# Optimization experiments

Measured on AMD Instinct MI355X. Metric: run time of the kernel, lower is better.

The kernel has to match this reference:

```python
import jax, jax.numpy as jnp
import numpy as np

ALPHA = 10.0
BETA = 2.0


def _l2norm(x):
    return x / jnp.linalg.norm(x, axis=1, keepdims=True)


def setup_inputs() -> dict:
    key = jax.random.key(0)
    k1, k2, k3 = jax.random.split(key, 3)
    n, C, d = 4096, 10000, 2048
    inputs = _l2norm(jax.random.normal(k1, (n, d), dtype=jnp.float32))
    kernel = _l2norm(jax.random.normal(k2, (C, d), dtype=jnp.float32))
    targets = jax.random.randint(k3, (n,), 0, C, dtype=jnp.int64 if jax.config.jax_enable_x64 else jnp.int32)
    return {"inputs": inputs, "targets": targets, "kernel": kernel}


def reference(inputs, targets, kernel):
    n = inputs.shape[0]
    C = kernel.shape[0]
    rows = jnp.arange(n)

    # cos_theta uses a detached kernel (no grad through this GEMM in original)
    cos = jnp.clip(inputs @ jax.lax.stop_gradient(kernel).T, -1.0, 1.0)  # [n, C]

    # phi_i = <inputs_i, kernel[targets_i]> - beta  (grad flows to kernel here)
    phi = jnp.sum(inputs * kernel[targets], axis=1) - BETA  # [n]

    pos_cos = cos[rows, targets]  # cos_theta at target columns, [n]
    mean_proxy_pos = pos_cos.sum() / n
    mean_proxy_neg = (cos.sum() - pos_cos.sum()) / (n * (C - 1))

    # output = cos_theta with target entries replaced by phi
    output = cos.at[rows, targets].set(phi)  # [n, C]
    onehot = jax.nn.one_hot(targets, C, dtype=output.dtype)

    loss_pos = phi  # sum(output * onehot, axis=1)
    loss_neg = jnp.log(jnp.sum(jnp.exp(output * ALPHA) * (1.0 - onehot), axis=1))  # [n]
    loss_mask = (jnp.max(output, axis=1) - phi) > 0.0
    per_sample = -loss_pos + loss_neg / ALPHA
    denom = jnp.maximum(loss_mask.sum(), 1).astype(per_sample.dtype)
    loss = jnp.sum(jnp.where(loss_mask, per_sample, 0.0)) / denom

    pred = jnp.argmax(output, axis=1)
    prec = jnp.mean((pred == targets).astype(jnp.float32))

    sim = inputs @ inputs.T  # [n, n]
    sim_label = (targets[:, None] == targets[None, :]).astype(sim.dtype)
    pos_cnt = sim_label.sum()
    neg_cnt = (n * n) - pos_cnt
    mean_pos_sim = jnp.sum(sim * sim_label) / pos_cnt
    mean_neg_sim = jnp.sum(sim * (1.0 - sim_label)) / neg_cnt

    return (loss, prec, mean_proxy_pos, mean_proxy_neg, mean_pos_sim, mean_neg_sim)
```

## Files before the change

### kernel.cpp

```cpp
#include <hip/hip_runtime.h>
#include <hip/hip_bf16.h>

#define NROWS 4096
#define NCLS  10000
#define DIM   2048
#define DIMB  1024
#define ALPHA_F 10.0f
#define BETA_F  2.0f
#define FP4_SCALE 64.0f
#define INVQ (1.0f / (FP4_SCALE * FP4_SCALE))
#define NMAIN_BLK 2560
#define NSIM_BLK  528

typedef float f32x4 __attribute__((ext_vector_type(4)));
typedef int   i32x4 __attribute__((ext_vector_type(4)));
typedef int   i32x8 __attribute__((ext_vector_type(8)));

__global__ void cast_fp4_kernel(const float* __restrict__ X, const float* __restrict__ Kn,
                                unsigned int* __restrict__ dA, unsigned int* __restrict__ dB,
                                int nA8, int nT8) {
  int stride = gridDim.x * blockDim.x;
  for (int i = blockIdx.x * blockDim.x + threadIdx.x; i < nT8; i += stride) {
    const float* src; unsigned int* dst; int j;
    if (i < nA8) { src = X; dst = dA; j = i; } else { src = Kn; dst = dB; j = i - nA8; }
    float4 a = reinterpret_cast<const float4*>(src)[2 * j];
    float4 b = reinterpret_cast<const float4*>(src)[2 * j + 1];
    float v[8] = {a.x, a.y, a.z, a.w, b.x, b.y, b.z, b.w};
    unsigned int w = 0;
#pragma unroll
    for (int q = 0; q < 8; ++q) {
      float s = v[q] * FP4_SCALE;
      float av = fabsf(s);
      unsigned int code = (unsigned)(av > 0.25f) + (av > 0.75f) + (av > 1.25f)
                        + (av > 1.75f) + (av > 2.5f) + (av > 3.5f) + (av > 5.0f);
      code |= (s < 0.f) ? 8u : 0u;
      w |= code << (4 * q);
    }
    dst[j] = w;
  }
}

__global__ void gather_dot_kernel(const float* __restrict__ X, const float* __restrict__ Kn,
                                  const int* __restrict__ tgt, float* __restrict__ dotv) {
  int gtid = blockIdx.x * blockDim.x + threadIdx.x;
  int wave = gtid >> 6;
  int lane = threadIdx.x & 63;
  if (wave >= NROWS) return;
  const float* xr = X + (size_t)wave * DIM;
  const float* kr = Kn + (size_t)tgt[wave] * DIM;
  float s = 0.f;
#pragma unroll
  for (int it = 0; it < DIM / 256; ++it) {
    int k = lane * 4 + it * 256;
    float4 a = *reinterpret_cast<const float4*>(xr + k);
    float4 b = *reinterpret_cast<const float4*>(kr + k);
    s += a.x * b.x + a.y * b.y + a.z * b.z + a.w * b.w;
  }
#pragma unroll
  for (int off = 32; off > 0; off >>= 1) s += __shfl_down(s, off);
  if (lane == 0) dotv[wave] = s;
}


#define AS1 const __attribute__((address_space(1))) void*
#define AS3 __attribute__((address_space(3))) void*

__global__ __launch_bounds__(256, 4)
void gemm_kernel(const unsigned char* __restrict__ A,
                 const unsigned char* __restrict__ Bm,
                 const float* __restrict__ dotv,
                 const int* __restrict__ tgt,
                 float* __restrict__ S1, float* __restrict__ Eacc,
                 float* __restrict__ CNT, float* __restrict__ simAcc) {
  __shared__ unsigned char lds[2 * 16384];

  const int tid  = threadIdx.x;
  const int lane = tid & 63;
  const int wid  = tid >> 6;
  const int wr   = wid >> 1;
  const int wc   = wid & 1;
  const int fr   = lane & 15;
  const int kg   = lane >> 4;

  const int lin = blockIdx.x;
  const bool isMain = lin < NMAIN_BLK;
  int rowTile, colTile, nB;
  const unsigned char* B;
  if (isMain) {
    int swz = (lin & 7) * 320 + (lin >> 3);
    colTile = swz / 32;
    rowTile = swz % 32;
    B = Bm; nB = NCLS;
  } else {
    int l2 = lin - NMAIN_BLK;
    int swz = (l2 & 7) * 66 + (l2 >> 3);
    int r = 0;
    while ((r + 1) * (r + 2) / 2 <= swz) ++r;
    rowTile = r;
    colTile = swz - r * (r + 1) / 2;
    B = A; nB = NROWS;
  }
  const int rowBase = rowTile * 128;
  const int colBase = colTile * 128;

  const int l0  = tid >> 3;
  const int sp  = tid & 7;
  const int lg8 = sp ^ (l0 & 7);
  const int shi = lg8 >> 2, sc16 = lg8 & 3;
  const int rA0 = rowBase + 2 * l0 + shi;
  const int rA1 = rA0 + 64;
  int cB0 = colBase + 2 * l0 + shi;      if (cB0 > nB - 1) cB0 = nB - 1;
  int cB1 = colBase + 64 + 2 * l0 + shi; if (cB1 > nB - 1) cB1 = nB - 1;
  const unsigned char* pA0 = A + (size_t)rA0 * DIMB + sc16 * 16;
  const unsigned char* pA1 = A + (size_t)rA1 * DIMB + sc16 * 16;
  const unsigned char* pB0 = B + (size_t)cB0 * DIMB + sc16 * 16;
  const unsigned char* pB1 = B + (size_t)cB1 * DIMB + sc16 * 16;
  const int dOff = l0 * 128 + sp * 16;

#define STAGE_TILE(BUF, KT)                                                     \
  { int ko_ = (KT) * 64;                                                        \
    unsigned char* d_ = lds + (BUF) * 16384 + dOff;                             \
    __builtin_amdgcn_global_load_lds((AS1)(pA0 + ko_), (AS3)(d_),          16, 0, 0); \
    __builtin_amdgcn_global_load_lds((AS1)(pA1 + ko_), (AS3)(d_ + 4096),   16, 0, 0); \
    __builtin_amdgcn_global_load_lds((AS1)(pB0 + ko_), (AS3)(d_ + 8192),   16, 0, 0); \
    __builtin_amdgcn_global_load_lds((AS1)(pB1 + ko_), (AS3)(d_ + 12288),  16, 0, 0); }

  int offA[4], offB[4];
#pragma unroll
  for (int m2 = 0; m2 < 4; ++m2) {
    int lr = wr * 64 + m2 * 16 + fr;
    int l = lr >> 1;
    offA[m2] = l * 128 + ((((lr & 1) * 4 + kg) ^ (l & 7)) << 4);
  }
#pragma unroll
  for (int n2 = 0; n2 < 4; ++n2) {
    int lc = wc * 64 + n2 * 16 + fr;
    int l = lc >> 1;
    offB[n2] = 8192 + l * 128 + ((((lc & 1) * 4 + kg) ^ (l & 7)) << 4);
  }

  f32x4 acc[4][4];
  const f32x4 zero = {0.f, 0.f, 0.f, 0.f};
#pragma unroll
  for (int m = 0; m < 4; ++m)
#pragma unroll
    for (int n = 0; n < 4; ++n) acc[m][n] = zero;

  STAGE_TILE(0, 0);
  __syncthreads();

#pragma unroll 1
  for (int kt = 0; kt < 16; ++kt) {
    const int buf = kt & 1;
    const int ktn = (kt < 15) ? kt + 1 : 15;
    STAGE_TILE(buf ^ 1, ktn);
    const unsigned char* lb = lds + buf * 16384;
    i32x8 afr[4], bfr[4];
#pragma unroll
    for (int m2 = 0; m2 < 4; ++m2) {
      i32x4 v_ = *reinterpret_cast<const i32x4*>(lb + offA[m2]);
      afr[m2][0] = v_[0]; afr[m2][1] = v_[1]; afr[m2][2] = v_[2]; afr[m2][3] = v_[3];
      afr[m2][4] = 0; afr[m2][5] = 0; afr[m2][6] = 0; afr[m2][7] = 0;
    }
#pragma unroll
    for (int n2 = 0; n2 < 4; ++n2) {
      i32x4 v_ = *reinterpret_cast<const i32x4*>(lb + offB[n2]);
      bfr[n2][0] = v_[0]; bfr[n2][1] = v_[1]; bfr[n2][2] = v_[2]; bfr[n2][3] = v_[3];
      bfr[n2][4] = 0; bfr[n2][5] = 0; bfr[n2][6] = 0; bfr[n2][7] = 0;
    }
    __builtin_amdgcn_s_setprio(1);
#pragma unroll
    for (int m2 = 0; m2 < 4; ++m2)
#pragma unroll
      for (int n2 = 0; n2 < 4; ++n2)
        acc[m2][n2] = __builtin_amdgcn_mfma_scale_f32_16x16x128_f8f6f4(
            afr[m2], bfr[n2], acc[m2][n2], 4, 4, 0, 127, 0, 127);
    __builtin_amdgcn_s_setprio(0);
    __syncthreads();
  }

  __syncthreads();

  if (isMain) {
    float* shPhi = reinterpret_cast<float*>(lds);
    if (tid < 128) shPhi[tid] = dotv[rowBase + tid] - BETA_F;
    __syncthreads();
#pragma unroll
    for (int m = 0; m < 4; ++m) {
#pragma unroll
      for (int j = 0; j < 4; ++j) {
        int rl = wr * 64 + m * 16 + kg * 4 + j;
        float ph = shPhi[rl];
        float s1 = 0.f, ee = 0.f, ct = 0.f;
#pragma unroll
        for (int n = 0; n < 4; ++n) {
          int gcol = colBase + wc * 64 + n * 16 + fr;
          float c = acc[m][n][j] * INVQ;
          c = fminf(fmaxf(c, -1.f), 1.f);
          if (gcol < NCLS) {
            s1 += c;
            ee += __expf(ALPHA_F * c);
            ct += (c > ph) ? 1.f : 0.f;
          }
        }
#pragma unroll
        for (int o = 1; o < 16; o <<= 1) {
          s1 += __shfl_xor(s1, o);
          ee += __shfl_xor(ee, o);
          ct += __shfl_xor(ct, o);
        }
        if (fr == 0) {
          int grow = rowBase + rl;
          atomicAdd(&S1[grow], s1);
          atomicAdd(&Eacc[grow], ee);
          atomicAdd(&CNT[grow], ct);
        }
      }
    }
  } else {
    const float wgt = (rowTile == colTile) ? 1.f : 2.f;
    int* shT = reinterpret_cast<int*>(lds);
    float* redbuf = reinterpret_cast<float*>(lds + 4096);
    if (tid < 128) shT[tid] = tgt[rowBase + tid];
    else if (tid < 256) shT[tid] = tgt[colBase + (tid - 128)];
    __syncthreads();
    float ps = 0.f, als = 0.f, pc = 0.f;
#pragma unroll
    for (int m = 0; m < 4; ++m) {
#pragma unroll
      for (int j = 0; j < 4; ++j) {
        int rl = wr * 64 + m * 16 + kg * 4 + j;
        int tr = shT[rl];
#pragma unroll
        for (int n = 0; n < 4; ++n) {
          int cl = wc * 64 + n * 16 + fr;
          float c = acc[m][n][j] * INVQ;
          als += c;
          if (tr == shT[128 + cl]) { ps += c; pc += 1.f; }
        }
      }
    }
#pragma unroll
    for (int o = 1; o < 64; o <<= 1) {
      ps  += __shfl_xor(ps, o);
      als += __shfl_xor(als, o);
      pc  += __shfl_xor(pc, o);
    }
    if (lane == 0) {
      redbuf[wid * 3 + 0] = ps;
      redbuf[wid * 3 + 1] = als;
      redbuf[wid * 3 + 2] = pc;
    }
    __syncthreads();
    if (tid == 0) {
      float p = 0.f, a = 0.f, c2 = 0.f;
      for (int w = 0; w < 4; ++w) {
        p += redbuf[w * 3 + 0];
        a += redbuf[w * 3 + 1];
        c2 += redbuf[w * 3 + 2];
      }
      atomicAdd(&simAcc[0], wgt * p);
      atomicAdd(&simAcc[1], wgt * a);
      atomicAdd(&simAcc[2], wgt * c2);
    }
  }
}

__global__ void finalize_kernel(const float* __restrict__ dotv, const float* __restrict__ S1,
                                const float* __restrict__ Eacc, const float* __restrict__ CNT,
                                const float* __restrict__ simAcc, float* __restrict__ out) {
  __shared__ float sh[5][256];
  int tid = threadIdx.x;
  float sum_posc = 0.f, sum_s1 = 0.f, loss_sum = 0.f, mask_cnt = 0.f, correct = 0.f;
  for (int i = tid; i < NROWS; i += 256) {
    float d = dotv[i];
    float posc = fminf(fmaxf(d, -1.f), 1.f);
    float phi = d - BETA_F;
    sum_posc += posc;
    sum_s1 += S1[i];
    float e = Eacc[i] - __expf(ALPHA_F * posc);
    float cexcl = CNT[i] - 1.f;
    float per = -phi + __logf(e) / ALPHA_F;
    if (cexcl > 0.5f) { loss_sum += per; mask_cnt += 1.f; }
    else correct += 1.f;
  }
  sh[0][tid] = sum_posc; sh[1][tid] = sum_s1; sh[2][tid] = loss_sum;
  sh[3][tid] = mask_cnt; sh[4][tid] = correct;
  __syncthreads();
  for (int s = 128; s > 0; s >>= 1) {
    if (tid < s)
      for (int q = 0; q < 5; ++q) sh[q][tid] += sh[q][tid + s];
    __syncthreads();
  }
  if (tid == 0) {
    float posS = sh[0][0], s1S = sh[1][0], lossS = sh[2][0], maskS = sh[3][0], corr = sh[4][0];
    out[0] = lossS / fmaxf(maskS, 1.f);
    out[1] = corr / (float)NROWS;
    out[2] = posS / (float)NROWS;
    out[3] = (s1S - posS) / ((float)NROWS * (float)(NCLS - 1));
    float pos = simAcc[0], all = simAcc[1], pcnt = simAcc[2];
    out[4] = pos / pcnt;
    out[5] = (all - pos) / ((float)NROWS * (float)NROWS - pcnt);
  }
}

extern "C" void kernel_launch(void* const* d_in, const int* in_sizes, int n_in,
                              void* d_out, int out_size, void* d_ws, size_t ws_size,
                              hipStream_t stream) {
  const float* X  = (const float*)d_in[0];
  const int*   tg = (const int*)d_in[1];
  const float* Kn = (const float*)d_in[2];
  float* out = (float*)d_out;

  char* w = (char*)d_ws;
  unsigned char* f4A = (unsigned char*)w;
  unsigned char* f4B = f4A + (size_t)NROWS * DIMB;
  float* dotv   = (float*)(w + (size_t)NROWS * DIMB + (size_t)NCLS * DIMB);
  float* S1     = dotv + NROWS;
  float* Eacc   = S1 + NROWS;
  float* CNT    = Eacc + NROWS;
  float* simAcc = CNT + NROWS;

  hipMemsetAsync(S1, 0, (3 * NROWS + 4) * sizeof(float), stream);

  const int nA8 = NROWS * DIM / 8, nT8 = nA8 + NCLS * DIM / 8;
  cast_fp4_kernel<<<2048, 256, 0, stream>>>(X, Kn, (unsigned int*)f4A,
                                            (unsigned int*)f4B, nA8, nT8);
  gather_dot_kernel<<<NROWS / 4, 256, 0, stream>>>(X, Kn, tg, dotv);

  gemm_kernel<<<NMAIN_BLK + NSIM_BLK, 256, 0, stream>>>(
      f4A, f4B, dotv, tg, S1, Eacc, CNT, simAcc);

  finalize_kernel<<<1, 256, 0, stream>>>(dotv, S1, Eacc, CNT, simAcc, out);
}
```

Before: 149.2 us.

## Fuse prep kernels, trim main grid, pack reductions, widen finalize

Merges the FP4 cast and gather-dot kernels into one launch, which saves a kernel launch and lets the two run concurrently. Shrinks the main GEMM grid from 2560 to 2528 blocks (79 column tiles × 32 row tiles cover 10112 ≥ 10000 columns) to drop fully out-of-range tiles. Hoists zero-initialisation of the fragment upper halves out of the k-loop. Packs the row sum and count into one float for the shuffle reduction, cutting one of the three shuffle chains at some risk to float precision. Runs finalize with 1024 threads instead of 256.

```diff
diff --git a/kernel.cpp b/kernel.cpp
--- a/kernel.cpp
+++ b/kernel.cpp
@@ -9,56 +9,56 @@
 #define BETA_F  2.0f
 #define FP4_SCALE 64.0f
 #define INVQ (1.0f / (FP4_SCALE * FP4_SCALE))
-#define NMAIN_BLK 2560
+#define NMAIN_BLK 2528
 #define NSIM_BLK  528
 
 typedef float f32x4 __attribute__((ext_vector_type(4)));
 typedef int   i32x4 __attribute__((ext_vector_type(4)));
 typedef int   i32x8 __attribute__((ext_vector_type(8)));
 
-__global__ void cast_fp4_kernel(const float* __restrict__ X, const float* __restrict__ Kn,
-                                unsigned int* __restrict__ dA, unsigned int* __restrict__ dB,
-                                int nA8, int nT8) {
-  int stride = gridDim.x * blockDim.x;
-  for (int i = blockIdx.x * blockDim.x + threadIdx.x; i < nT8; i += stride) {
-    const float* src; unsigned int* dst; int j;
-    if (i < nA8) { src = X; dst = dA; j = i; } else { src = Kn; dst = dB; j = i - nA8; }
-    float4 a = reinterpret_cast<const float4*>(src)[2 * j];
-    float4 b = reinterpret_cast<const float4*>(src)[2 * j + 1];
-    float v[8] = {a.x, a.y, a.z, a.w, b.x, b.y, b.z, b.w};
-    unsigned int w = 0;
-#pragma unroll
-    for (int q = 0; q < 8; ++q) {
-      float s = v[q] * FP4_SCALE;
-      float av = fabsf(s);
-      unsigned int code = (unsigned)(av > 0.25f) + (av > 0.75f) + (av > 1.25f)
-                        + (av > 1.75f) + (av > 2.5f) + (av > 3.5f) + (av > 5.0f);
-      code |= (s < 0.f) ? 8u : 0u;
-      w |= code << (4 * q);
-    }
-    dst[j] = w;
-  }
-}
-
-__global__ void gather_dot_kernel(const float* __restrict__ X, const float* __restrict__ Kn,
-                                  const int* __restrict__ tgt, float* __restrict__ dotv) {
-  int gtid = blockIdx.x * blockDim.x + threadIdx.x;
-  int wave = gtid >> 6;
-  int lane = threadIdx.x & 63;
-  if (wave >= NROWS) return;
-  const float* xr = X + (size_t)wave * DIM;
-  const float* kr = Kn + (size_t)tgt[wave] * DIM;
-  float s = 0.f;
-#pragma unroll
-  for (int it = 0; it < DIM / 256; ++it) {
-    int k = lane * 4 + it * 256;
-    float4 a = *reinterpret_cast<const float4*>(xr + k);
-    float4 b = *reinterpret_cast<const float4*>(kr + k);
-    s += a.x * b.x + a.y * b.y + a.z * b.z + a.w * b.w;
-  }
-#pragma unroll
-  for (int off = 32; off > 0; off >>= 1) s += __shfl_down(s, off);
-  if (lane == 0) dotv[wave] = s;
+__global__ void prep_kernel(const float* __restrict__ X, const float* __restrict__ Kn,
+                            const int* __restrict__ tgt,
+                            unsigned int* __restrict__ dA, unsigned int* __restrict__ dB,
+                            float* __restrict__ dotv, int nA8, int nT8) {
+  if (blockIdx.x < 2048) {
+    int stride = 2048 * blockDim.x;
+    for (int i = blockIdx.x * blockDim.x + threadIdx.x; i < nT8; i += stride) {
+      const float* src; unsigned int* dst; int j;
+      if (i < nA8) { src = X; dst = dA; j = i; } else { src = Kn; dst = dB; j = i - nA8; }
+      float4 a = reinterpret_cast<const float4*>(src)[2 * j];
+      float4 b = reinterpret_cast<const float4*>(src)[2 * j + 1];
+      float v[8] = {a.x, a.y, a.z, a.w, b.x, b.y, b.z, b.w};
+      unsigned int w = 0;
+#pragma unroll
+      for (int q = 0; q < 8; ++q) {
+        float s = v[q] * FP4_SCALE;
+        float av = fabsf(s);
+        unsigned int code = (unsigned)(av > 0.25f) + (av > 0.75f) + (av > 1.25f)
+                          + (av > 1.75f) + (av > 2.5f) + (av > 3.5f) + (av > 5.0f);
+        code |= (s < 0.f) ? 8u : 0u;
+        w |= code << (4 * q);
+      }
+      dst[j] = w;
+    }
+  } else {
+    int gtid = (blockIdx.x - 2048) * blockDim.x + threadIdx.x;
+    int wave = gtid >> 6;
+    int lane = threadIdx.x & 63;
+    if (wave >= NROWS) return;
+    const float* xr = X + (size_t)wave * DIM;
+    const float* kr = Kn + (size_t)tgt[wave] * DIM;
+    float s = 0.f;
+#pragma unroll
+    for (int it = 0; it < DIM / 256; ++it) {
+      int k = lane * 4 + it * 256;
+      float4 a = *reinterpret_cast<const float4*>(xr + k);
+      float4 b = *reinterpret_cast<const float4*>(kr + k);
+      s += a.x * b.x + a.y * b.y + a.z * b.z + a.w * b.w;
+    }
+#pragma unroll
+    for (int off = 32; off > 0; off >>= 1) s += __shfl_down(s, off);
+    if (lane == 0) dotv[wave] = s;
+  }
 }
 
 
@@ -87,7 +87,7 @@
   int rowTile, colTile, nB;
   const unsigned char* B;
   if (isMain) {
-    int swz = (lin & 7) * 320 + (lin >> 3);
+    int swz = (lin & 7) * 316 + (lin >> 3);
     colTile = swz / 32;
     rowTile = swz % 32;
     B = Bm; nB = NCLS;
@@ -146,6 +146,13 @@
 #pragma unroll
     for (int n = 0; n < 4; ++n) acc[m][n] = zero;
 
+  i32x8 afr[4], bfr[4];
+#pragma unroll
+  for (int q = 0; q < 4; ++q) {
+#pragma unroll
+    for (int e = 0; e < 8; ++e) { afr[q][e] = 0; bfr[q][e] = 0; }
+  }
+
   STAGE_TILE(0, 0);
   __syncthreads();
 
@@ -155,18 +162,15 @@
     const int ktn = (kt < 15) ? kt + 1 : 15;
     STAGE_TILE(buf ^ 1, ktn);
     const unsigned char* lb = lds + buf * 16384;
-    i32x8 afr[4], bfr[4];
 #pragma unroll
     for (int m2 = 0; m2 < 4; ++m2) {
       i32x4 v_ = *reinterpret_cast<const i32x4*>(lb + offA[m2]);
       afr[m2][0] = v_[0]; afr[m2][1] = v_[1]; afr[m2][2] = v_[2]; afr[m2][3] = v_[3];
-      afr[m2][4] = 0; afr[m2][5] = 0; afr[m2][6] = 0; afr[m2][7] = 0;
     }
 #pragma unroll
     for (int n2 = 0; n2 < 4; ++n2) {
       i32x4 v_ = *reinterpret_cast<const i32x4*>(lb + offB[n2]);
       bfr[n2][0] = v_[0]; bfr[n2][1] = v_[1]; bfr[n2][2] = v_[2]; bfr[n2][3] = v_[3];
-      bfr[n2][4] = 0; bfr[n2][5] = 0; bfr[n2][6] = 0; bfr[n2][7] = 0;
     }
     __builtin_amdgcn_s_setprio(1);
 #pragma unroll
@@ -203,17 +207,19 @@
             ct += (c > ph) ? 1.f : 0.f;
           }
         }
+        float pk = s1 + ct * 4096.0f;
 #pragma unroll
         for (int o = 1; o < 16; o <<= 1) {
-          s1 += __shfl_xor(s1, o);
+          pk += __shfl_xor(pk, o);
           ee += __shfl_xor(ee, o);
-          ct += __shfl_xor(ct, o);
         }
         if (fr == 0) {
           int grow = rowBase + rl;
-          atomicAdd(&S1[grow], s1);
+          float ctv = rintf(pk * (1.0f / 4096.0f));
+          float s1v = pk - ctv * 4096.0f;
+          atomicAdd(&S1[grow], s1v);
           atomicAdd(&Eacc[grow], ee);
-          atomicAdd(&CNT[grow], ct);
+          atomicAdd(&CNT[grow], ctv);
         }
       }
     }
@@ -269,10 +275,10 @@
 __global__ void finalize_kernel(const float* __restrict__ dotv, const float* __restrict__ S1,
                                 const float* __restrict__ Eacc, const float* __restrict__ CNT,
                                 const float* __restrict__ simAcc, float* __restrict__ out) {
-  __shared__ float sh[5][256];
+  __shared__ float sh[5][1024];
   int tid = threadIdx.x;
   float sum_posc = 0.f, sum_s1 = 0.f, loss_sum = 0.f, mask_cnt = 0.f, correct = 0.f;
-  for (int i = tid; i < NROWS; i += 256) {
+  for (int i = tid; i < NROWS; i += 1024) {
     float d = dotv[i];
     float posc = fminf(fmaxf(d, -1.f), 1.f);
     float phi = d - BETA_F;
@@ -287,7 +293,7 @@
   sh[0][tid] = sum_posc; sh[1][tid] = sum_s1; sh[2][tid] = loss_sum;
   sh[3][tid] = mask_cnt; sh[4][tid] = correct;
   __syncthreads();
-  for (int s = 128; s > 0; s >>= 1) {
+  for (int s = 512; s > 0; s >>= 1) {
     if (tid < s)
       for (int q = 0; q < 5; ++q) sh[q][tid] += sh[q][tid + s];
     __syncthreads();
@@ -324,12 +330,11 @@
   hipMemsetAsync(S1, 0, (3 * NROWS + 4) * sizeof(float), stream);
 
   const int nA8 = NROWS * DIM / 8, nT8 = nA8 + NCLS * DIM / 8;
-  cast_fp4_kernel<<<2048, 256, 0, stream>>>(X, Kn, (unsigned int*)f4A,
-                                            (unsigned int*)f4B, nA8, nT8);
-  gather_dot_kernel<<<NROWS / 4, 256, 0, stream>>>(X, Kn, tg, dotv);
+  prep_kernel<<<3072, 256, 0, stream>>>(X, Kn, tg, (unsigned int*)f4A,
+                                        (unsigned int*)f4B, dotv, nA8, nT8);
 
   gemm_kernel<<<NMAIN_BLK + NSIM_BLK, 256, 0, stream>>>(
       f4A, f4B, dotv, tg, S1, Eacc, CNT, simAcc);
 
-  finalize_kernel<<<1, 256, 0, stream>>>(dotv, S1, Eacc, CNT, simAcc, out);
+  finalize_kernel<<<1, 1024, 0, stream>>>(dotv, S1, Eacc, CNT, simAcc, out);
 }
```

Result: faster. 134.8 us (median of 2 runs) (-9.7%).
